# Optimization experiments

Measured on AMD Instinct MI355X. Metric: run time of the kernel, lower is better.

Reference implementation:

```python
import jax, jax.numpy as jnp
import numpy as np

HEADS = 16
DIM_HEAD = 64
EPS = 1e-8
MASK_VALUE = -np.finfo(np.float32).max


def rotate_half(x):
    # x: [..., rot_dim]; split into two halves (j=2 grouping) and rotate
    x1, x2 = jnp.split(x.reshape(*x.shape[:-1], 2, x.shape[-1] // 2), 2, axis=-2)
    x1 = x1.squeeze(-2)
    x2 = x2.squeeze(-2)
    return jnp.concatenate((-x2, x1), axis=-1)


def apply_rotary_pos_emb(t, freqs):
    # t: [b, h, n, d], freqs: [n, rot_dim]
    rot_dim = freqs.shape[-1]
    t_rot, t_pass = t[..., :rot_dim], t[..., rot_dim:]
    t_rot = t_rot * jnp.cos(freqs) + rotate_half(t_rot) * jnp.sin(freqs)
    return jnp.concatenate((t_rot, t_pass), axis=-1)


def setup_inputs() -> dict:
    key = jax.random.key(0)
    ks = jax.random.split(key, 6)
    b, n, dim = 2, 2048, 1024
    inner = HEADS * DIM_HEAD
    rot_dim = 32
    return {
        "x": jax.random.normal(ks[0], (b, n, dim), jnp.float32),
        "freqs": jax.random.normal(ks[1], (n, rot_dim), jnp.float32),
        "gamma": jnp.ones((dim,), jnp.float32),
        "Wq": jax.random.normal(ks[2], (dim, inner), jnp.float32) * (dim ** -0.5),
        "Wkv": jax.random.normal(ks[3], (dim, 2 * inner), jnp.float32) * (dim ** -0.5),
        "Wo": jax.random.normal(ks[4], (inner, dim), jnp.float32) * (inner ** -0.5),
        "bo": jnp.zeros((dim,), jnp.float32),
    }


def reference(x, freqs, gamma, Wq, Wkv, Wo, bo):
    b, n, dim = x.shape
    scale = DIM_HEAD ** -0.5

    # RMSNorm (norm-based formulation, matching the torch code)
    norm = jnp.linalg.norm(x, axis=-1, keepdims=True) * (dim ** -0.5)
    xn = x / jnp.maximum(norm, EPS) * gamma

    q = xn @ Wq                      # [b, n, h*d]
    kv = xn @ Wkv                    # [b, n, 2*h*d]
    k, v = jnp.split(kv, 2, axis=-1)

    def to_heads(t):
        return t.reshape(b, n, HEADS, DIM_HEAD).transpose(0, 2, 1, 3)  # [b,h,n,d]

    q, k, v = map(to_heads, (q, k, v))
    q = q * scale

    q = apply_rotary_pos_emb(q, freqs)
    k = apply_rotary_pos_emb(k, freqs)

    sim = jnp.einsum('bhid,bhjd->bhij', q, k)
    causal_mask = jnp.triu(jnp.ones((n, n), bool), k=1)
    sim = jnp.where(causal_mask, MASK_VALUE, sim)

    attn = jax.nn.softmax(sim, axis=-1)
    out = jnp.einsum('bhij,bhjd->bhid', attn, v)
    out = out.transpose(0, 2, 1, 3).reshape(b, n, HEADS * DIM_HEAD)
    return out @ Wo + bo
```

## Files before the change

### kernel.cpp

```cpp
#include <hip/hip_runtime.h>
#include <hip/hip_bf16.h>
#include <math.h>

typedef short s8 __attribute__((ext_vector_type(8)));
typedef float f4 __attribute__((ext_vector_type(4)));

#define HEADS 16
#define DHEAD 64
#define NSEQ 2048
#define BATCH 2
#define DIM 1024
#define ROT 32
#define QSCALE 0.18033688011112042f

static __device__ __forceinline__ unsigned short f2bf(float f) {
    union { float f; unsigned int u; } v; v.f = f;
    unsigned int u = v.u;
    unsigned int r = (u + 0x7FFFu + ((u >> 16) & 1u)) >> 16;
    return (unsigned short)r;
}

static __device__ __forceinline__ unsigned int cvt_pk_bf16(float lo, float hi) {
    unsigned int r;
    asm volatile("v_cvt_pk_bf16_f32 %0, %1, %2" : "=v"(r) : "v"(lo), "v"(hi));
    return r;
}

static __device__ __forceinline__ void gload_lds16(
        const unsigned short* g, unsigned short* l) {
    __builtin_amdgcn_global_load_lds(
        (const __attribute__((address_space(1))) void*)g,
        (__attribute__((address_space(3))) void*)l,
        16, 0, 0);
}

static __device__ __forceinline__ void tr_tile(
        const float* __restrict__ in, unsigned short* __restrict__ out,
        int K, int N, int n0, int k0, int tid, float* tile ) {
    int tx = tid & 31, ty = tid >> 5;
    #pragma unroll
    for (int j = 0; j < 32; j += 8)
        tile[(ty + j) * 33 + tx] = in[(size_t)(k0 + ty + j) * N + n0 + tx];
    __syncthreads();
    #pragma unroll
    for (int j = 0; j < 32; j += 8)
        out[(size_t)(n0 + ty + j) * K + k0 + tx] = f2bf(tile[tx * 33 + ty + j]);
}

__global__ __launch_bounds__(256) void prep_kernel(
        const float* __restrict__ Wq, const float* __restrict__ Wkv,
        const float* __restrict__ Wo, const float* __restrict__ freqs,
        unsigned short* __restrict__ WqT, unsigned short* __restrict__ WkvT,
        unsigned short* __restrict__ WoT, float* __restrict__ cs) {
    __shared__ float tile[32 * 33];
    int bid = blockIdx.x, tid = threadIdx.x;
    if (bid < 1024) {
        tr_tile(Wq, WqT, 1024, 1024, (bid & 31) * 32, (bid >> 5) * 32, tid, tile);
    } else if (bid < 3072) {
        int idx = bid - 1024;
        tr_tile(Wkv, WkvT, 1024, 2048, (idx & 63) * 32, (idx >> 6) * 32, tid, tile);
    } else if (bid < 4096) {
        int idx = bid - 3072;
        tr_tile(Wo, WoT, 1024, 1024, (idx & 31) * 32, (idx >> 5) * 32, tid, tile);
    } else {
        int i = (bid - 4096) * 256 + tid;
        int npos = i >> 6, j = i & 63;
        int q = j >> 4;
        int fi = (q >> 1) * 16 + (j & 15);
        float f = freqs[npos * ROT + fi];
        cs[i] = (q & 1) ? sinf(f) : cosf(f);
    }
}

__global__ __launch_bounds__(256) void rmsnorm_kernel(
        const float* __restrict__ x, const float* __restrict__ gamma,
        unsigned short* __restrict__ xn) {
    int row = blockIdx.x;
    int tid = threadIdx.x;
    float4 v = ((const float4*)(x + (size_t)row * DIM))[tid];
    float ss = v.x * v.x + v.y * v.y + v.z * v.z + v.w * v.w;
    #pragma unroll
    for (int m = 1; m < 64; m <<= 1) ss += __shfl_xor(ss, m, 64);
    __shared__ float wsum[4];
    int wave = tid >> 6;
    if ((tid & 63) == 0) wsum[wave] = ss;
    __syncthreads();
    float total = wsum[0] + wsum[1] + wsum[2] + wsum[3];
    float norm = sqrtf(total * (1.0f / DIM));
    float inv = 1.0f / fmaxf(norm, 1e-8f);
    float4 g = ((const float4*)gamma)[tid];
    ushort4 o;
    o.x = f2bf(v.x * inv * g.x);
    o.y = f2bf(v.y * inv * g.y);
    o.z = f2bf(v.z * inv * g.z);
    o.w = f2bf(v.w * inv * g.w);
    ((ushort4*)(xn + (size_t)row * DIM))[tid] = o;
}

static __device__ __forceinline__ void gemm_core64(
        const unsigned short* __restrict__ A, const unsigned short* __restrict__ BT,
        int bm0, int bn0, unsigned short* As, unsigned short* Bs, f4 acc[2][4]) {
    const int Kd = DIM;
    int tid = threadIdx.x, lane = tid & 63, w = tid >> 6;
    int wr = w >> 1, wc = w & 1;
    int r16 = lane & 15, g8 = 8 * (lane >> 4);
    int srow = lane >> 2, scol = (lane & 3) * 8;
    const unsigned short* Ag0 = A  + (size_t)(bm0 + w * 16 + srow) * Kd + scol;
    const unsigned short* Bg0 = BT + (size_t)(bn0 + (w * 2 + 0) * 16 + srow) * Kd + scol;
    const unsigned short* Bg1 = BT + (size_t)(bn0 + (w * 2 + 1) * 16 + srow) * Kd + scol;
    unsigned short* Al  = As + w * 512;
    unsigned short* Bl0 = Bs + (w * 2 + 0) * 512;
    unsigned short* Bl1 = Bs + (w * 2 + 1) * 512;
    const unsigned short* ar = As + (wr * 32 + r16) * 32 + g8;
    const unsigned short* br = Bs + (wc * 64 + r16) * 32 + g8;
    for (int k0 = 0; k0 < Kd; k0 += 32) {
        gload_lds16(Ag0 + k0, Al);
        gload_lds16(Bg0 + k0, Bl0);
        gload_lds16(Bg1 + k0, Bl1);
        __syncthreads();
        s8 a0 = *(const s8*)(ar);
        s8 a1 = *(const s8*)(ar + 512);
        s8 b0 = *(const s8*)(br);
        s8 b1 = *(const s8*)(br + 512);
        s8 b2 = *(const s8*)(br + 1024);
        s8 b3 = *(const s8*)(br + 1536);
        acc[0][0] = __builtin_amdgcn_mfma_f32_16x16x32_bf16(a0, b0, acc[0][0], 0, 0, 0);
        acc[0][1] = __builtin_amdgcn_mfma_f32_16x16x32_bf16(a0, b1, acc[0][1], 0, 0, 0);
        acc[0][2] = __builtin_amdgcn_mfma_f32_16x16x32_bf16(a0, b2, acc[0][2], 0, 0, 0);
        acc[0][3] = __builtin_amdgcn_mfma_f32_16x16x32_bf16(a0, b3, acc[0][3], 0, 0, 0);
        acc[1][0] = __builtin_amdgcn_mfma_f32_16x16x32_bf16(a1, b0, acc[1][0], 0, 0, 0);
        acc[1][1] = __builtin_amdgcn_mfma_f32_16x16x32_bf16(a1, b1, acc[1][1], 0, 0, 0);
        acc[1][2] = __builtin_amdgcn_mfma_f32_16x16x32_bf16(a1, b2, acc[1][2], 0, 0, 0);
        acc[1][3] = __builtin_amdgcn_mfma_f32_16x16x32_bf16(a1, b3, acc[1][3], 0, 0, 0);
        __syncthreads();
    }
}

__global__ __launch_bounds__(256) void gemm_qkv(
        const unsigned short* __restrict__ xn, const unsigned short* __restrict__ WqT,
        const unsigned short* __restrict__ WkvT, const float* __restrict__ cs,
        unsigned short* __restrict__ q_h, unsigned short* __restrict__ k_h,
        unsigned short* __restrict__ v_t) {
    __shared__ unsigned short As[64 * 32];
    __shared__ unsigned short Bs[128 * 32];
    f4 acc[2][4];
    #pragma unroll
    for (int m = 0; m < 2; ++m)
        #pragma unroll
        for (int n = 0; n < 4; ++n) acc[m][n] = 0.f;
    int bx = blockIdx.x;
    bool isq = (bx < 8);
    int bm0 = blockIdx.y * 64;
    int bn0 = (isq ? bx : (bx - 8)) * 128;
    gemm_core64(xn, isq ? WqT : WkvT, bm0, bn0, As, Bs, acc);
    int lane = threadIdx.x & 63, w = threadIdx.x >> 6;
    int wr = w >> 1, wc = w & 1, g = lane >> 4, c0 = lane & 15;
    if (isq) {
        int h = 2 * bx + wc;
        #pragma unroll
        for (int m = 0; m < 2; ++m)
            #pragma unroll
            for (int r = 0; r < 4; ++r) {
                int row = bm0 + wr * 32 + m * 16 + 4 * g + r;
                int b = row >> 11, npos = row & 2047;
                const float* csr = cs + npos * 64;
                float a0 = acc[m][0][r] * QSCALE;
                float a1 = acc[m][1][r] * QSCALE;
                float q0 = a0 * csr[c0] - a1 * csr[16 + c0];
                float q1 = a1 * csr[32 + c0] + a0 * csr[48 + c0];
                unsigned short* dst = q_h + ((size_t)(b * HEADS + h) * NSEQ + npos) * DHEAD;
                dst[c0]      = f2bf(q0);
                dst[16 + c0] = f2bf(q1);
                dst[32 + c0] = f2bf(acc[m][2][r] * QSCALE);
                dst[48 + c0] = f2bf(acc[m][3][r] * QSCALE);
            }
    } else if (bx < 16) {
        int h = 2 * (bx - 8) + wc;
        #pragma unroll
        for (int m = 0; m < 2; ++m)
            #pragma unroll
            for (int r = 0; r < 4; ++r) {
                int row = bm0 + wr * 32 + m * 16 + 4 * g + r;
                int b = row >> 11, npos = row & 2047;
                const float* csr = cs + npos * 64;
                float a0 = acc[m][0][r], a1 = acc[m][1][r];
                float k0v = a0 * csr[c0] - a1 * csr[16 + c0];
                float k1v = a1 * csr[32 + c0] + a0 * csr[48 + c0];
                unsigned short* dst = k_h + ((size_t)(b * HEADS + h) * NSEQ + npos) * DHEAD;
                dst[c0]      = f2bf(k0v);
                dst[16 + c0] = f2bf(k1v);
                dst[32 + c0] = f2bf(acc[m][2][r]);
                dst[48 + c0] = f2bf(acc[m][3][r]);
            }
    } else {
        int h = 2 * (bx - 16) + wc;
        #pragma unroll
        for (int m = 0; m < 2; ++m) {
            int row0 = bm0 + wr * 32 + m * 16 + 4 * g;
            int b = row0 >> 11, npos0 = row0 & 2047;
            unsigned short* vb = v_t + (size_t)(b * HEADS + h) * DHEAD * NSEQ;
            #pragma unroll
            for (int n = 0; n < 4; ++n) {
                uint2 pk;
                pk.x = cvt_pk_bf16(acc[m][n][0], acc[m][n][1]);
                pk.y = cvt_pk_bf16(acc[m][n][2], acc[m][n][3]);
                *(uint2*)(vb + (size_t)(n * 16 + c0) * NSEQ + npos0) = pk;
            }
        }
    }
}

#define PSTRIDE 72

static __device__ __forceinline__ void stage_kv64(
        const unsigned short* __restrict__ kb, const unsigned short* __restrict__ vb,
        int j0, unsigned short* Kd, unsigned short* Vd, int w, int lane) {
    int r8 = lane >> 3, c = lane & 7;
    int sc = c ^ r8;
    #pragma unroll
    for (int i = 0; i < 2; ++i) {
        int rb = (w * 2 + i) * 8;
        int r = rb + r8;
        gload_lds16(kb + (size_t)(j0 + r) * DHEAD + sc * 8, Kd + rb * DHEAD);
        gload_lds16(vb + (size_t)r * NSEQ + j0 + sc * 8,    Vd + rb * DHEAD);
    }
}

template<bool MASKT>
static __device__ __forceinline__ void attn_tile_lds(
        int j0, int q0, int g, int c0, int njt,
        const unsigned short* Kc, const unsigned short* Vc,
        s8 qf0, s8 qf1, unsigned short* plw,
        f4 o[4], float& m, float& l) {
    int sw = c0 & 7;
    int off0 = ((g ^ sw) << 3);
    int off1 = (((g + 4) ^ sw) << 3);
    f4 s[4];
    #pragma unroll
    for (int jt = 0; jt < 4; ++jt) {
        f4 acc; acc = 0.f;
        if (!MASKT || jt < njt) {
            const unsigned short* kp = Kc + (jt * 16 + c0) * DHEAD;
            s8 kf0 = *(const s8*)(kp + off0);
            s8 kf1 = *(const s8*)(kp + off1);
            acc = __builtin_amdgcn_mfma_f32_16x16x32_bf16(kf0, qf0, acc, 0, 0, 0);
            acc = __builtin_amdgcn_mfma_f32_16x16x32_bf16(kf1, qf1, acc, 0, 0, 0);
        }
        s[jt] = acc;
    }
    if (MASKT) {
        #pragma unroll
        for (int jt = 0; jt < 4; ++jt)
            #pragma unroll
            for (int r = 0; r < 4; ++r) {
                int j = j0 + jt * 16 + 4 * g + r;
                if (j > q0 + c0) s[jt][r] = -1e30f;
            }
    }
    f4 mv = s[0];
    #pragma unroll
    for (int jt = 1; jt < 4; ++jt)
        #pragma unroll
        for (int r = 0; r < 4; ++r) mv[r] = fmaxf(mv[r], s[jt][r]);
    float mx = fmaxf(fmaxf(mv[0], mv[1]), fmaxf(mv[2], mv[3]));
    mx = fmaxf(mx, __shfl_xor(mx, 16));
    mx = fmaxf(mx, __shfl_xor(mx, 32));
    if (__any(mx > m + 11.5f)) {
        float mnew = fmaxf(m, mx);
        float alpha = exp2f(m - mnew);
        l *= alpha;
        #pragma unroll
        for (int dc = 0; dc < 4; ++dc)
            #pragma unroll
            for (int r = 0; r < 4; ++r) o[dc][r] *= alpha;
        m = mnew;
    }
    float rs = 0.f;
    unsigned int* prow = (unsigned int*)(plw + c0 * PSTRIDE);
    #pragma unroll
    for (int jt = 0; jt < 4; ++jt) {
        f4 p;
        #pragma unroll
        for (int r = 0; r < 4; ++r) { p[r] = exp2f(s[jt][r] - m); rs += p[r]; }
        uint2 pk;
        pk.x = cvt_pk_bf16(p[0], p[1]);
        pk.y = cvt_pk_bf16(p[2], p[3]);
        ((uint2*)prow)[jt * 4 + g] = pk;
    }
    rs += __shfl_xor(rs, 16);
    rs += __shfl_xor(rs, 32);
    l += rs;
    __builtin_amdgcn_sched_barrier(0);
    asm volatile("s_waitcnt lgkmcnt(0)" ::: "memory");
    __builtin_amdgcn_sched_barrier(0);
    const unsigned short* prd = plw + c0 * PSTRIDE + 8 * g;
    s8 pf0 = *(const s8*)(prd);
    s8 pf1 = *(const s8*)(prd + 32);
    bool hi_half = (!MASKT) || (njt > 2);
    #pragma unroll
    for (int dc = 0; dc < 4; ++dc) {
        const unsigned short* vp = Vc + (dc * 16 + c0) * DHEAD;
        s8 vf0 = *(const s8*)(vp + off0);
        o[dc] = __builtin_amdgcn_mfma_f32_16x16x32_bf16(vf0, pf0, o[dc], 0, 0, 0);
        if (hi_half) {
            s8 vf1 = *(const s8*)(vp + off1);
            o[dc] = __builtin_amdgcn_mfma_f32_16x16x32_bf16(vf1, pf1, o[dc], 0, 0, 0);
        }
    }
}

__global__ __launch_bounds__(256) void attn_kernel(
        const unsigned short* __restrict__ q_h, const unsigned short* __restrict__ k_h,
        const unsigned short* __restrict__ v_t, unsigned short* __restrict__ attn_out) {
    __shared__ unsigned short Ks[2][64 * DHEAD];
    __shared__ unsigned short Vs[2][64 * DHEAD];
    __shared__ unsigned short p_lds[4][16][PSTRIDE];
    int tid = threadIdx.x, lane = tid & 63, w = tid >> 6;
    int g = lane >> 4, c0 = lane & 15;
    int bid = blockIdx.x;
    int k = bid >> 3;
    int qt = 31 - (k >> 2);
    int bh = (bid & 7) + ((k & 3) << 3);
    const unsigned short* qb = q_h + (size_t)bh * NSEQ * DHEAD;
    const unsigned short* kb = k_h + (size_t)bh * NSEQ * DHEAD;
    const unsigned short* vb = v_t + (size_t)bh * DHEAD * NSEQ;
    unsigned short* plw = &p_lds[w][0][0];
    int b = bh >> 4, h = bh & 15;
    int q0 = qt * 64 + w * 16;
    s8 qf0 = *(const s8*)(qb + (size_t)(q0 + c0) * DHEAD + 8 * g);
    s8 qf1 = *(const s8*)(qb + (size_t)(q0 + c0) * DHEAD + 32 + 8 * g);
    f4 o[4]; o[0] = 0.f; o[1] = 0.f; o[2] = 0.f; o[3] = 0.f;
    float m = -1e30f, l = 0.f;
    int nt = qt + 1;
    stage_kv64(kb, vb, 0, Ks[0], Vs[0], w, lane);
    __syncthreads();
    for (int t = 0; t < nt; ++t) {
        const unsigned short* Kc = Ks[t & 1];
        const unsigned short* Vc = Vs[t & 1];
        if (t + 1 < nt)
            stage_kv64(kb, vb, (t + 1) * 64, Ks[(t + 1) & 1], Vs[(t + 1) & 1], w, lane);
        if (t == nt - 1)
            attn_tile_lds<true>(t * 64, q0, g, c0, w + 1, Kc, Vc, qf0, qf1, plw, o, m, l);
        else
            attn_tile_lds<false>(t * 64, q0, g, c0, 4, Kc, Vc, qf0, qf1, plw, o, m, l);
        __syncthreads();
    }
    float invl = 1.0f / l;
    unsigned short* dst = attn_out + ((size_t)(b * NSEQ) + q0 + c0) * (HEADS * DHEAD) + h * DHEAD;
    #pragma unroll
    for (int dc = 0; dc < 4; ++dc) {
        uint2 pk;
        pk.x = cvt_pk_bf16(o[dc][0] * invl, o[dc][1] * invl);
        pk.y = cvt_pk_bf16(o[dc][2] * invl, o[dc][3] * invl);
        *(uint2*)(dst + dc * 16 + 4 * g) = pk;
    }
}

__global__ __launch_bounds__(256) void gemm_o(
        const unsigned short* __restrict__ attn, const unsigned short* __restrict__ WoT,
        const float* __restrict__ bo, float* __restrict__ out) {
    __shared__ unsigned short As[64 * 32];
    __shared__ unsigned short Bs[128 * 32];
    f4 acc[2][4];
    #pragma unroll
    for (int m = 0; m < 2; ++m)
        #pragma unroll
        for (int n = 0; n < 4; ++n) acc[m][n] = 0.f;
    int bm0 = blockIdx.y * 64, bn0 = blockIdx.x * 128;
    gemm_core64(attn, WoT, bm0, bn0, As, Bs, acc);
    int lane = threadIdx.x & 63, w = threadIdx.x >> 6;
    int wr = w >> 1, wc = w & 1, g = lane >> 4, c0 = lane & 15;
    #pragma unroll
    for (int m = 0; m < 2; ++m)
        #pragma unroll
        for (int r = 0; r < 4; ++r) {
            int row = bm0 + wr * 32 + m * 16 + 4 * g + r;
            #pragma unroll
            for (int n = 0; n < 4; ++n) {
                int col = bn0 + wc * 64 + n * 16 + c0;
                out[(size_t)row * DIM + col] = acc[m][n][r] + bo[col];
            }
        }
}

extern "C" void kernel_launch(void* const* d_in, const int* in_sizes, int n_in,
                              void* d_out, int out_size, void* d_ws, size_t ws_size,
                              hipStream_t stream) {
    const float* x     = (const float*)d_in[0];
    const float* freqs = (const float*)d_in[1];
    const float* gamma = (const float*)d_in[2];
    const float* Wq    = (const float*)d_in[3];
    const float* Wkv   = (const float*)d_in[4];
    const float* Wo    = (const float*)d_in[5];
    const float* bo    = (const float*)d_in[6];
    float* out = (float*)d_out;

    char* ws = (char*)d_ws;
    unsigned short* xn   = (unsigned short*)(ws + 0);
    unsigned short* WqT  = (unsigned short*)(ws + 8388608);
    unsigned short* WkvT = (unsigned short*)(ws + 10485760);
    unsigned short* WoT  = (unsigned short*)(ws + 14680064);
    unsigned short* q_h  = (unsigned short*)(ws + 16777216);
    unsigned short* k_h  = (unsigned short*)(ws + 25165824);
    unsigned short* v_t  = (unsigned short*)(ws + 33554432);
    float*          cs   = (float*)(ws + 41943040);
    unsigned short* attn = xn;

    prep_kernel<<<4608, 256, 0, stream>>>(Wq, Wkv, Wo, freqs, WqT, WkvT, WoT, cs);
    rmsnorm_kernel<<<4096, 256, 0, stream>>>(x, gamma, xn);
    gemm_qkv<<<dim3(24, 64), 256, 0, stream>>>(xn, WqT, WkvT, cs, q_h, k_h, v_t);
    attn_kernel<<<1024, 256, 0, stream>>>(q_h, k_h, v_t, attn);
    gemm_o  <<<dim3(8, 64), 256, 0, stream>>>(attn, WoT, bo, out);
}
```

Baseline: 128.9 us.

## Double-buffer GEMM LDS tiles and merge RMSNorm into prep kernel

```diff
diff --git a/kernel.cpp b/kernel.cpp
--- a/kernel.cpp
+++ b/kernel.cpp
@@ -47,23 +47,45 @@
         out[(size_t)(n0 + ty + j) * K + k0 + tx] = f2bf(tile[tx * 33 + ty + j]);
 }
 
-__global__ __launch_bounds__(256) void prep_kernel(
+__global__ __launch_bounds__(256) void prep_rms_kernel(
+        const float* __restrict__ x, const float* __restrict__ gamma,
         const float* __restrict__ Wq, const float* __restrict__ Wkv,
         const float* __restrict__ Wo, const float* __restrict__ freqs,
-        unsigned short* __restrict__ WqT, unsigned short* __restrict__ WkvT,
-        unsigned short* __restrict__ WoT, float* __restrict__ cs) {
-    __shared__ float tile[32 * 33];
+        unsigned short* __restrict__ xn, unsigned short* __restrict__ WqT,
+        unsigned short* __restrict__ WkvT, unsigned short* __restrict__ WoT,
+        float* __restrict__ cs) {
+    __shared__ float smem[32 * 33];
     int bid = blockIdx.x, tid = threadIdx.x;
-    if (bid < 1024) {
-        tr_tile(Wq, WqT, 1024, 1024, (bid & 31) * 32, (bid >> 5) * 32, tid, tile);
-    } else if (bid < 3072) {
-        int idx = bid - 1024;
-        tr_tile(Wkv, WkvT, 1024, 2048, (idx & 63) * 32, (idx >> 6) * 32, tid, tile);
-    } else if (bid < 4096) {
-        int idx = bid - 3072;
-        tr_tile(Wo, WoT, 1024, 1024, (idx & 31) * 32, (idx >> 5) * 32, tid, tile);
+    if (bid < 4096) {
+        int row = bid;
+        float4 v = ((const float4*)(x + (size_t)row * DIM))[tid];
+        float ss = v.x * v.x + v.y * v.y + v.z * v.z + v.w * v.w;
+        #pragma unroll
+        for (int m = 1; m < 64; m <<= 1) ss += __shfl_xor(ss, m, 64);
+        int wave = tid >> 6;
+        if ((tid & 63) == 0) smem[wave] = ss;
+        __syncthreads();
+        float total = smem[0] + smem[1] + smem[2] + smem[3];
+        float norm = sqrtf(total * (1.0f / DIM));
+        float inv = 1.0f / fmaxf(norm, 1e-8f);
+        float4 g = ((const float4*)gamma)[tid];
+        ushort4 o;
+        o.x = f2bf(v.x * inv * g.x);
+        o.y = f2bf(v.y * inv * g.y);
+        o.z = f2bf(v.z * inv * g.z);
+        o.w = f2bf(v.w * inv * g.w);
+        ((ushort4*)(xn + (size_t)row * DIM))[tid] = o;
+    } else if (bid < 5120) {
+        int idx = bid - 4096;
+        tr_tile(Wq, WqT, 1024, 1024, (idx & 31) * 32, (idx >> 5) * 32, tid, smem);
+    } else if (bid < 7168) {
+        int idx = bid - 5120;
+        tr_tile(Wkv, WkvT, 1024, 2048, (idx & 63) * 32, (idx >> 6) * 32, tid, smem);
+    } else if (bid < 8192) {
+        int idx = bid - 7168;
+        tr_tile(Wo, WoT, 1024, 1024, (idx & 31) * 32, (idx >> 5) * 32, tid, smem);
     } else {
-        int i = (bid - 4096) * 256 + tid;
+        int i = (bid - 8192) * 256 + tid;
         int npos = i >> 6, j = i & 63;
         int q = j >> 4;
         int fi = (q >> 1) * 16 + (j & 15);
@@ -72,32 +94,30 @@
     }
 }
 
-__global__ __launch_bounds__(256) void rmsnorm_kernel(
-        const float* __restrict__ x, const float* __restrict__ gamma,
-        unsigned short* __restrict__ xn) {
-    int row = blockIdx.x;
-    int tid = threadIdx.x;
-    float4 v = ((const float4*)(x + (size_t)row * DIM))[tid];
-    float ss = v.x * v.x + v.y * v.y + v.z * v.z + v.w * v.w;
-    #pragma unroll
-    for (int m = 1; m < 64; m <<= 1) ss += __shfl_xor(ss, m, 64);
-    __shared__ float wsum[4];
-    int wave = tid >> 6;
-    if ((tid & 63) == 0) wsum[wave] = ss;
-    __syncthreads();
-    float total = wsum[0] + wsum[1] + wsum[2] + wsum[3];
-    float norm = sqrtf(total * (1.0f / DIM));
-    float inv = 1.0f / fmaxf(norm, 1e-8f);
-    float4 g = ((const float4*)gamma)[tid];
-    ushort4 o;
-    o.x = f2bf(v.x * inv * g.x);
-    o.y = f2bf(v.y * inv * g.y);
-    o.z = f2bf(v.z * inv * g.z);
-    o.w = f2bf(v.w * inv * g.w);
-    ((ushort4*)(xn + (size_t)row * DIM))[tid] = o;
-}
-
-static __device__ __forceinline__ void gemm_core64(
+#define GEMM_COMPUTE(AOFF, BOFF)                                                        \
+    {                                                                                   \
+        s8 a0 = *(const s8*)(ar + (AOFF));                                              \
+        s8 a1 = *(const s8*)(ar + (AOFF) + 512);                                        \
+        s8 b0 = *(const s8*)(br + (BOFF));                                              \
+        s8 b1 = *(const s8*)(br + (BOFF) + 512);                                        \
+        s8 b2 = *(const s8*)(br + (BOFF) + 1024);                                       \
+        s8 b3 = *(const s8*)(br + (BOFF) + 1536);                                       \
+        acc[0][0] = __builtin_amdgcn_mfma_f32_16x16x32_bf16(a0, b0, acc[0][0], 0, 0, 0);\
+        acc[0][1] = __builtin_amdgcn_mfma_f32_16x16x32_bf16(a0, b1, acc[0][1], 0, 0, 0);\
+        acc[0][2] = __builtin_amdgcn_mfma_f32_16x16x32_bf16(a0, b2, acc[0][2], 0, 0, 0);\
+        acc[0][3] = __builtin_amdgcn_mfma_f32_16x16x32_bf16(a0, b3, acc[0][3], 0, 0, 0);\
+        acc[1][0] = __builtin_amdgcn_mfma_f32_16x16x32_bf16(a1, b0, acc[1][0], 0, 0, 0);\
+        acc[1][1] = __builtin_amdgcn_mfma_f32_16x16x32_bf16(a1, b1, acc[1][1], 0, 0, 0);\
+        acc[1][2] = __builtin_amdgcn_mfma_f32_16x16x32_bf16(a1, b2, acc[1][2], 0, 0, 0);\
+        acc[1][3] = __builtin_amdgcn_mfma_f32_16x16x32_bf16(a1, b3, acc[1][3], 0, 0, 0);\
+    }
+
+#define GEMM_FENCE()                                             \
+    asm volatile("s_waitcnt vmcnt(0)" ::: "memory");             \
+    __builtin_amdgcn_s_barrier();                                \
+    __builtin_amdgcn_sched_barrier(0);
+
+static __device__ __forceinline__ void gemm_core64_db(
         const unsigned short* __restrict__ A, const unsigned short* __restrict__ BT,
         int bm0, int bn0, unsigned short* As, unsigned short* Bs, f4 acc[2][4]) {
     const int Kd = DIM;
@@ -113,26 +133,27 @@
     unsigned short* Bl1 = Bs + (w * 2 + 1) * 512;
     const unsigned short* ar = As + (wr * 32 + r16) * 32 + g8;
     const unsigned short* br = Bs + (wc * 64 + r16) * 32 + g8;
-    for (int k0 = 0; k0 < Kd; k0 += 32) {
-        gload_lds16(Ag0 + k0, Al);
-        gload_lds16(Bg0 + k0, Bl0);
-        gload_lds16(Bg1 + k0, Bl1);
-        __syncthreads();
-        s8 a0 = *(const s8*)(ar);
-        s8 a1 = *(const s8*)(ar + 512);
-        s8 b0 = *(const s8*)(br);
-        s8 b1 = *(const s8*)(br + 512);
-        s8 b2 = *(const s8*)(br + 1024);
-        s8 b3 = *(const s8*)(br + 1536);
-        acc[0][0] = __builtin_amdgcn_mfma_f32_16x16x32_bf16(a0, b0, acc[0][0], 0, 0, 0);
-        acc[0][1] = __builtin_amdgcn_mfma_f32_16x16x32_bf16(a0, b1, acc[0][1], 0, 0, 0);
-        acc[0][2] = __builtin_amdgcn_mfma_f32_16x16x32_bf16(a0, b2, acc[0][2], 0, 0, 0);
-        acc[0][3] = __builtin_amdgcn_mfma_f32_16x16x32_bf16(a0, b3, acc[0][3], 0, 0, 0);
-        acc[1][0] = __builtin_amdgcn_mfma_f32_16x16x32_bf16(a1, b0, acc[1][0], 0, 0, 0);
-        acc[1][1] = __builtin_amdgcn_mfma_f32_16x16x32_bf16(a1, b1, acc[1][1], 0, 0, 0);
-        acc[1][2] = __builtin_amdgcn_mfma_f32_16x16x32_bf16(a1, b2, acc[1][2], 0, 0, 0);
-        acc[1][3] = __builtin_amdgcn_mfma_f32_16x16x32_bf16(a1, b3, acc[1][3], 0, 0, 0);
-        __syncthreads();
+    gload_lds16(Ag0, Al);
+    gload_lds16(Bg0, Bl0);
+    gload_lds16(Bg1, Bl1);
+    GEMM_FENCE();
+    for (int t = 0; t < 32; t += 2) {
+        {
+            int k1 = (t + 1) * 32;
+            gload_lds16(Ag0 + k1, Al + 2048);
+            gload_lds16(Bg0 + k1, Bl0 + 4096);
+            gload_lds16(Bg1 + k1, Bl1 + 4096);
+        }
+        GEMM_COMPUTE(0, 0);
+        GEMM_FENCE();
+        if (t + 2 < 32) {
+            int k2 = (t + 2) * 32;
+            gload_lds16(Ag0 + k2, Al);
+            gload_lds16(Bg0 + k2, Bl0);
+            gload_lds16(Bg1 + k2, Bl1);
+        }
+        GEMM_COMPUTE(2048, 4096);
+        GEMM_FENCE();
     }
 }
 
@@ -141,8 +162,8 @@
         const unsigned short* __restrict__ WkvT, const float* __restrict__ cs,
         unsigned short* __restrict__ q_h, unsigned short* __restrict__ k_h,
         unsigned short* __restrict__ v_t) {
-    __shared__ unsigned short As[64 * 32];
-    __shared__ unsigned short Bs[128 * 32];
+    __shared__ unsigned short As[2 * 64 * 32];
+    __shared__ unsigned short Bs[2 * 128 * 32];
     f4 acc[2][4];
     #pragma unroll
     for (int m = 0; m < 2; ++m)
@@ -152,7 +173,7 @@
     bool isq = (bx < 8);
     int bm0 = blockIdx.y * 64;
     int bn0 = (isq ? bx : (bx - 8)) * 128;
-    gemm_core64(xn, isq ? WqT : WkvT, bm0, bn0, As, Bs, acc);
+    gemm_core64_db(xn, isq ? WqT : WkvT, bm0, bn0, As, Bs, acc);
     int lane = threadIdx.x & 63, w = threadIdx.x >> 6;
     int wr = w >> 1, wc = w & 1, g = lane >> 4, c0 = lane & 15;
     if (isq) {
@@ -359,15 +380,15 @@
 __global__ __launch_bounds__(256) void gemm_o(
         const unsigned short* __restrict__ attn, const unsigned short* __restrict__ WoT,
         const float* __restrict__ bo, float* __restrict__ out) {
-    __shared__ unsigned short As[64 * 32];
-    __shared__ unsigned short Bs[128 * 32];
+    __shared__ unsigned short As[2 * 64 * 32];
+    __shared__ unsigned short Bs[2 * 128 * 32];
     f4 acc[2][4];
     #pragma unroll
     for (int m = 0; m < 2; ++m)
         #pragma unroll
         for (int n = 0; n < 4; ++n) acc[m][n] = 0.f;
     int bm0 = blockIdx.y * 64, bn0 = blockIdx.x * 128;
-    gemm_core64(attn, WoT, bm0, bn0, As, Bs, acc);
+    gemm_core64_db(attn, WoT, bm0, bn0, As, Bs, acc);
     int lane = threadIdx.x & 63, w = threadIdx.x >> 6;
     int wr = w >> 1, wc = w & 1, g = lane >> 4, c0 = lane & 15;
     #pragma unroll
@@ -406,8 +427,8 @@
     float*          cs   = (float*)(ws + 41943040);
     unsigned short* attn = xn;
 
-    prep_kernel<<<4608, 256, 0, stream>>>(Wq, Wkv, Wo, freqs, WqT, WkvT, WoT, cs);
-    rmsnorm_kernel<<<4096, 256, 0, stream>>>(x, gamma, xn);
+    prep_rms_kernel<<<8704, 256, 0, stream>>>(x, gamma, Wq, Wkv, Wo, freqs,
+                                              xn, WqT, WkvT, WoT, cs);
     gemm_qkv<<<dim3(24, 64), 256, 0, stream>>>(xn, WqT, WkvT, cs, q_h, k_h, v_t);
     attn_kernel<<<1024, 256, 0, stream>>>(q_h, k_h, v_t, attn);
     gemm_o  <<<dim3(8, 64), 256, 0, stream>>>(attn, WoT, bo, out);
```

Result: slower. 133.6 us (+3.6%).
